# Optimization experiments

Hardware: AMD Instinct MI355X
Metric: run time of the kernel (lower is better)

The kernel has to match this reference:

```python
import jax, jax.numpy as jnp
import numpy as np

B = 512
D_IN = 64
D_MODEL = 768
DEPTH = 24
D_INNER = 1536   # expand=2 * d_model
D_STATE = 16
D_CONV = 4
DT_RANK = 48     # ceil(d_model/16)


def setup_inputs() -> dict:
    key = jax.random.key(0)
    ks = jax.random.split(key, 12)
    s = 0.02
    x_t = jax.random.normal(ks[0], (B, 1, D_IN), dtype=jnp.float32)
    in_w = jax.random.normal(ks[1], (D_MODEL, D_IN), dtype=jnp.float32) * s
    in_b = jnp.zeros((D_MODEL,), jnp.float32)
    xz_w = jax.random.normal(ks[2], (DEPTH, 2 * D_INNER, D_MODEL), dtype=jnp.float32) * s
    conv_w = jax.random.normal(ks[3], (DEPTH, D_INNER, D_CONV), dtype=jnp.float32) * s
    conv_b = jnp.zeros((DEPTH, D_INNER), jnp.float32)
    xproj_w = jax.random.normal(ks[4], (DEPTH, DT_RANK + 2 * D_STATE, D_INNER), dtype=jnp.float32) * s
    dtproj_w = jax.random.normal(ks[5], (DEPTH, D_INNER, DT_RANK), dtype=jnp.float32) * s
    # dt bias initialized so softplus(dt) ~ [1e-3, 1e-1], as in mamba_ssm
    dtproj_b = jax.random.uniform(ks[6], (DEPTH, D_INNER), minval=-4.6, maxval=-2.3)
    # A = arange(1, d_state+1) per channel -> A_log = log(A)
    A_log = jnp.broadcast_to(jnp.log(jnp.arange(1, D_STATE + 1, dtype=jnp.float32)),
                             (DEPTH, D_INNER, D_STATE)).copy()
    D = jnp.ones((DEPTH, D_INNER), jnp.float32)
    outproj_w = jax.random.normal(ks[7], (DEPTH, D_MODEL, D_INNER), dtype=jnp.float32) * s
    conv_state = jax.random.normal(ks[8], (DEPTH, B, D_INNER, D_CONV), dtype=jnp.float32) * 0.1
    ssm_state = jax.random.normal(ks[9], (DEPTH, B, D_INNER, D_STATE), dtype=jnp.float32) * 0.1
    ln_g = jnp.ones((D_MODEL,), jnp.float32)
    ln_b = jnp.zeros((D_MODEL,), jnp.float32)
    return dict(x_t=x_t, in_w=in_w, in_b=in_b, xz_w=xz_w, conv_w=conv_w, conv_b=conv_b,
                xproj_w=xproj_w, dtproj_w=dtproj_w, dtproj_b=dtproj_b, A_log=A_log, D=D,
                outproj_w=outproj_w, conv_state=conv_state, ssm_state=ssm_state,
                ln_g=ln_g, ln_b=ln_b)


def _layer_step(h, layer):
    """One Mamba selective-scan decode step for a single layer. h: (B, D_INNER*... wait (B, d_model))"""
    (xz_w, conv_w, conv_b, xproj_w, dtproj_w, dtproj_b, A_log, Dp, outproj_w, cs, ss) = layer
    xz = h @ xz_w.T                                  # (B, 2*d_inner)
    x, z = jnp.split(xz, 2, axis=-1)                 # (B, d_inner) each
    # causal conv1d cache update: shift left, append new token
    cs = jnp.concatenate([cs[..., 1:], x[..., None]], axis=-1)   # (B, d_inner, d_conv)
    x = jnp.sum(cs * conv_w[None], axis=-1) + conv_b             # (B, d_inner)
    x = jax.nn.silu(x)
    xdb = x @ xproj_w.T                              # (B, dt_rank + 2*d_state)
    dt = xdb[:, :DT_RANK] @ dtproj_w.T               # (B, d_inner)
    Bm = xdb[:, DT_RANK:DT_RANK + D_STATE]           # (B, d_state)
    C = xdb[:, DT_RANK + D_STATE:]                   # (B, d_state)
    dt = jax.nn.softplus(dt + dtproj_b)
    A = -jnp.exp(A_log)                              # (d_inner, d_state)
    dA = jnp.exp(dt[:, :, None] * A[None])           # (B, d_inner, d_state)
    ss = ss * dA + (dt * x)[:, :, None] * Bm[:, None, :]
    y = jnp.einsum('bdn,bn->bd', ss, C) + Dp * x
    y = y * jax.nn.silu(z)
    h = y @ outproj_w.T                              # (B, d_model)
    return h, None


def reference(x_t, in_w, in_b, xz_w, conv_w, conv_b, xproj_w, dtproj_w, dtproj_b,
              A_log, D, outproj_w, conv_state, ssm_state, ln_g, ln_b):
    h = x_t[:, 0, :] @ in_w.T + in_b                 # (B, d_model)
    h, _ = jax.lax.scan(_layer_step, h,
                        (xz_w, conv_w, conv_b, xproj_w, dtproj_w, dtproj_b,
                         A_log, D, outproj_w, conv_state, ssm_state))
    mu = jnp.mean(h, axis=-1, keepdims=True)
    var = jnp.var(h, axis=-1, keepdims=True)
    h = (h - mu) / jnp.sqrt(var + 1e-5) * ln_g + ln_b
    return h[:, None, :]                             # (B, 1, d_model)
```

## Files before the change

kernel.cpp:

```cpp
#include <hip/hip_runtime.h>
#include <cstdint>
#include <cstddef>

#define BATCH 512
#define D_IN 64
#define D_MODEL 768
#define DEPTH 24
#define D_INNER 1536
#define D_STATE 16
#define D_CONV 4
#define DT_RANK 48
#define XDB_DIM 80

typedef __bf16 bf16x8 __attribute__((ext_vector_type(8)));
typedef unsigned short ushortx8 __attribute__((ext_vector_type(8)));
typedef float f32x4 __attribute__((ext_vector_type(4)));
typedef unsigned short ushort_t;

#define XZW_N ((size_t)2 * D_INNER * D_MODEL)
#define OPW_N ((size_t)D_MODEL * D_INNER)
#define XZ_ALL ((long)DEPTH * (long)(XZW_N / 8))
#define OP_ALL ((long)DEPTH * (long)(OPW_N / 8))
#define AN_ALL ((long)DEPTH * D_INNER * D_STATE / 8)

__device__ __forceinline__ float sigmoidf_(float v) { return 1.f / (1.f + __expf(-v)); }

__device__ __forceinline__ void split1(float f, unsigned short& h, unsigned short& l) {
    unsigned int u = __float_as_uint(f);
    unsigned int uh = u & 0xffff0000u;
    h = (unsigned short)(uh >> 16);
    float r = f - __uint_as_float(uh);
    l = (unsigned short)(__float_as_uint(r) >> 16);
}

__device__ __forceinline__ void split8(const float* s, ushort_t* hi, ushort_t* lo) {
    float4 A4 = *(const float4*)s;
    float4 B4 = *(const float4*)(s + 4);
    float f[8] = {A4.x, A4.y, A4.z, A4.w, B4.x, B4.y, B4.z, B4.w};
    ushortx8 h, l;
#pragma unroll
    for (int j = 0; j < 8; ++j) {
        unsigned short hh, ll;
        split1(f[j], hh, ll);
        h[j] = hh; l[j] = ll;
    }
    *(ushortx8*)hi = h;
    *(ushortx8*)lo = l;
}

__global__ __launch_bounds__(256) void k_prep(
    const float* __restrict__ xz_w, const float* __restrict__ op_w,
    const float* __restrict__ A_log,
    ushort_t* __restrict__ xzw_hi, ushort_t* __restrict__ xzw_lo,
    ushort_t* __restrict__ opw_hi, ushort_t* __restrict__ opw_lo,
    float* __restrict__ Aneg)
{
    const long total = XZ_ALL + OP_ALL + AN_ALL;
    long g = (long)blockIdx.x * 256 + threadIdx.x;
    const long stride = (long)gridDim.x * 256;
    for (; g < total; g += stride) {
        if (g < XZ_ALL) {
            split8(xz_w + g * 8, xzw_hi + g * 8, xzw_lo + g * 8);
        } else if (g < XZ_ALL + OP_ALL) {
            const long r = g - XZ_ALL;
            split8(op_w + r * 8, opw_hi + r * 8, opw_lo + r * 8);
        } else {
            const long r = g - XZ_ALL - OP_ALL;
            const float* s = A_log + r * 8;
            float* d = Aneg + r * 8;
#pragma unroll
            for (int j = 0; j < 8; ++j) d[j] = -__expf(s[j]);
        }
    }
}

__global__ __launch_bounds__(256) void k_inproj(
    const float* __restrict__ A, const float* __restrict__ W,
    const float* __restrict__ bias,
    ushort_t* __restrict__ Chi, ushort_t* __restrict__ Clo)
{
    __shared__ float As[16][68];
    __shared__ float Ws[16][68];
    const int tid = threadIdx.x;
    const int tx = tid & 15, ty = tid >> 4;
    const int bn0 = blockIdx.x * 64, bm0 = blockIdx.y * 64;
    float acc[4][4] = {};
    for (int k0 = 0; k0 < D_IN; k0 += 16) {
        int r = tid >> 2, c = (tid & 3) << 2;
        float4 a4 = *(const float4*)(A + (size_t)(bm0 + r) * D_IN + k0 + c);
        As[c + 0][r] = a4.x; As[c + 1][r] = a4.y;
        As[c + 2][r] = a4.z; As[c + 3][r] = a4.w;
        float4 w4 = *(const float4*)(W + (size_t)(bn0 + r) * D_IN + k0 + c);
        Ws[c + 0][r] = w4.x; Ws[c + 1][r] = w4.y;
        Ws[c + 2][r] = w4.z; Ws[c + 3][r] = w4.w;
        __syncthreads();
#pragma unroll
        for (int kk = 0; kk < 16; ++kk) {
            float af[4], wf[4];
#pragma unroll
            for (int i = 0; i < 4; ++i) af[i] = As[kk][ty * 4 + i];
#pragma unroll
            for (int j = 0; j < 4; ++j) wf[j] = Ws[kk][tx * 4 + j];
#pragma unroll
            for (int i = 0; i < 4; ++i)
#pragma unroll
                for (int j = 0; j < 4; ++j) acc[i][j] += af[i] * wf[j];
        }
        __syncthreads();
    }
#pragma unroll
    for (int i = 0; i < 4; ++i) {
        const int bb = bm0 + ty * 4 + i;
#pragma unroll
        for (int j = 0; j < 4; ++j) {
            const int n = bn0 + tx * 4 + j;
            float v = acc[i][j] + bias[n];
            const size_t idx = (size_t)bb * D_MODEL + n;
            unsigned short hh, ll;
            split1(v, hh, ll);
            Chi[idx] = hh;
            Clo[idx] = ll;
        }
    }
}

template<int MODE>
__global__ __launch_bounds__(256) void k_gemm(
    const ushort_t* __restrict__ Ahi, const ushort_t* __restrict__ Alo,
    const ushort_t* __restrict__ Whi, const ushort_t* __restrict__ Wlo,
    float* __restrict__ xout, float* __restrict__ gout,
    float* __restrict__ hout, ushort_t* __restrict__ Chi, ushort_t* __restrict__ Clo,
    const float* __restrict__ conv_state, const float* __restrict__ conv_w,
    const float* __restrict__ conv_b)
{
    constexpr int K = (MODE == 0) ? D_MODEL : D_INNER;
    constexpr int nk = K / 32;
    const int bid = blockIdx.x;
    int c, r;
    if (MODE == 0) {
        c = (bid & 7) + ((bid >> 6) << 3);
        r = (bid >> 3) & 7;
    } else {
        if (bid < 64) { c = bid & 7; r = bid >> 3; }
        else { const int j = bid - 64; c = 8 + (j & 3); r = j >> 2; }
    }
    const int bn0 = c * 64, bm0 = r * 64;

    __shared__ __align__(16) unsigned short As[2][64 * 64];
    __shared__ __align__(16) unsigned short Bs[2][64 * 64];

    const int t = threadIdx.x;
    const int sr = t >> 2, s0 = t & 3;
    const int lane = t & 63, wv = t >> 6;
    const int wm = wv >> 1, wn = wv & 1;
    const int ln15 = lane & 15, kq = lane >> 4;

    const ushort_t* Ah = Ahi + (size_t)(bm0 + sr) * K + s0 * 8;
    const ushort_t* Al = Alo + (size_t)(bm0 + sr) * K + s0 * 8;
    const ushort_t* Wh = Whi + (size_t)(bn0 + sr) * K + s0 * 8;
    const ushort_t* Wl = Wlo + (size_t)(bn0 + sr) * K + s0 * 8;

    f32x4 acc[2][2];
#pragma unroll
    for (int m = 0; m < 2; ++m)
#pragma unroll
        for (int n = 0; n < 2; ++n) acc[m][n] = (f32x4){0.f, 0.f, 0.f, 0.f};

    const int sw = sr & 7;
    auto stage = [&](ushortx8 hi, ushortx8 lo, unsigned short* S) {
        *(ushortx8*)&S[sr * 64 + ((s0 ^ sw) << 3)] = hi;
        *(ushortx8*)&S[sr * 64 + (((s0 + 4) ^ sw) << 3)] = lo;
    };

    ushortx8 pah = *(const ushortx8*)Ah;
    ushortx8 pal = *(const ushortx8*)Al;
    ushortx8 pwh = *(const ushortx8*)Wh;
    ushortx8 pwl = *(const ushortx8*)Wl;
    stage(pah, pal, As[0]);
    stage(pwh, pwl, Bs[0]);

    for (int kb = 0; kb < nk; ++kb) {
        __syncthreads();
        const int cur = kb & 1;
        if (kb + 1 < nk) {
            const int ko = (kb + 1) << 5;
            pah = *(const ushortx8*)(Ah + ko);
            pal = *(const ushortx8*)(Al + ko);
            pwh = *(const ushortx8*)(Wh + ko);
            pwl = *(const ushortx8*)(Wl + ko);
        }
        bf16x8 ah[2], al2[2], bh[2], bl[2];
#pragma unroll
        for (int m = 0; m < 2; ++m) {
            const int rr = wm * 32 + m * 16 + ln15;
            const int base = rr * 64;
            const int rs = rr & 7;
            ah[m]  = __builtin_bit_cast(bf16x8, *(ushortx8*)&As[cur][base + ((kq ^ rs) << 3)]);
            al2[m] = __builtin_bit_cast(bf16x8, *(ushortx8*)&As[cur][base + (((kq + 4) ^ rs) << 3)]);
        }
#pragma unroll
        for (int n = 0; n < 2; ++n) {
            const int rr = wn * 32 + n * 16 + ln15;
            const int base = rr * 64;
            const int rs = rr & 7;
            bh[n] = __builtin_bit_cast(bf16x8, *(ushortx8*)&Bs[cur][base + ((kq ^ rs) << 3)]);
            bl[n] = __builtin_bit_cast(bf16x8, *(ushortx8*)&Bs[cur][base + (((kq + 4) ^ rs) << 3)]);
        }
#pragma unroll
        for (int m = 0; m < 2; ++m)
#pragma unroll
            for (int n = 0; n < 2; ++n) {
                acc[m][n] = __builtin_amdgcn_mfma_f32_16x16x32_bf16(ah[m],  bh[n], acc[m][n], 0, 0, 0);
                acc[m][n] = __builtin_amdgcn_mfma_f32_16x16x32_bf16(ah[m],  bl[n], acc[m][n], 0, 0, 0);
                acc[m][n] = __builtin_amdgcn_mfma_f32_16x16x32_bf16(al2[m], bh[n], acc[m][n], 0, 0, 0);
            }
        if (kb + 1 < nk) {
            stage(pah, pal, As[cur ^ 1]);
            stage(pwh, pwl, Bs[cur ^ 1]);
        }
    }

#pragma unroll
    for (int m = 0; m < 2; ++m) {
#pragma unroll
        for (int n = 0; n < 2; ++n) {
            const int col = bn0 + wn * 32 + n * 16 + ln15;
            const int row0 = bm0 + wm * 32 + m * 16 + kq * 4;
            f32x4 v = acc[m][n];
            if (MODE == 0) {
                if (col < D_INNER) {
                    const float4 cwv = *(const float4*)(conv_w + (size_t)col * 4);
                    const float cbv = conv_b[col];
#pragma unroll
                    for (int j = 0; j < 4; ++j) {
                        const int row = row0 + j;
                        const float4 csv = *(const float4*)(conv_state + ((size_t)row * D_INNER + col) * 4);
                        float cc = csv.y * cwv.x + csv.z * cwv.y + csv.w * cwv.z
                                 + v[j] * cwv.w + cbv;
                        xout[(size_t)row * D_INNER + col] = cc * sigmoidf_(cc);
                    }
                } else {
#pragma unroll
                    for (int j = 0; j < 4; ++j) {
                        float zv = v[j];
                        gout[(size_t)(row0 + j) * D_INNER + (col - D_INNER)] = zv * sigmoidf_(zv);
                    }
                }
            } else {
#pragma unroll
                for (int j = 0; j < 4; ++j) {
                    const size_t idx = (size_t)(row0 + j) * D_MODEL + col;
                    float val = v[j];
                    hout[idx] = val;
                    unsigned short hh, ll;
                    split1(val, hh, ll);
                    Chi[idx] = hh;
                    Clo[idx] = ll;
                }
            }
        }
    }
}

__global__ __launch_bounds__(256) void k_bc(
    const float* __restrict__ x, const float* __restrict__ g,
    const float* __restrict__ xproj_w, const float* __restrict__ dtproj_w,
    const float* __restrict__ dtproj_b, const float* __restrict__ Aneg_l,
    const float* __restrict__ Dp, const float* __restrict__ ssm,
    ushort_t* __restrict__ yhi, ushort_t* __restrict__ ylo)
{
    __shared__ __align__(16) float xs0[D_INNER];
    __shared__ __align__(16) float xs1[D_INNER];
    __shared__ float xdb0[XDB_DIM];
    __shared__ float xdb1[XDB_DIM];
    const int tid = threadIdx.x;
    const int b0 = blockIdx.x * 2, b1 = b0 + 1;

    {
        const float4* xr0 = (const float4*)(x + (size_t)b0 * D_INNER);
        const float4* xr1 = (const float4*)(x + (size_t)b1 * D_INNER);
        float4* d0 = (float4*)xs0; float4* d1 = (float4*)xs1;
        for (int i = tid; i < D_INNER / 4; i += 256) { d0[i] = xr0[i]; d1[i] = xr1[i]; }
    }
    __syncthreads();

    const int lane = tid & 63, wv = tid >> 6;
    const float4* xs40 = (const float4*)xs0;
    const float4* xs41 = (const float4*)xs1;
    for (int n = wv; n < XDB_DIM; n += 4) {
        const float4* wr = (const float4*)(xproj_w + (size_t)n * D_INNER);
        float s0 = 0.f, s1 = 0.f;
#pragma unroll
        for (int j = 0; j < D_INNER / 4 / 64; ++j) {
            float4 w = wr[lane + 64 * j];
            float4 u = xs40[lane + 64 * j];
            float4 q = xs41[lane + 64 * j];
            s0 += w.x * u.x + w.y * u.y + w.z * u.z + w.w * u.w;
            s1 += w.x * q.x + w.y * q.y + w.z * q.z + w.w * q.w;
        }
#pragma unroll
        for (int off = 32; off > 0; off >>= 1) { s0 += __shfl_xor(s0, off); s1 += __shfl_xor(s1, off); }
        if (lane == 0) { xdb0[n] = s0; xdb1[n] = s1; }
    }
    __syncthreads();

    float B0[16], C0[16], B1[16], C1[16];
#pragma unroll
    for (int n = 0; n < 16; ++n) {
        B0[n] = xdb0[DT_RANK + n]; C0[n] = xdb0[DT_RANK + 16 + n];
        B1[n] = xdb1[DT_RANK + n]; C1[n] = xdb1[DT_RANK + 16 + n];
    }

    for (int d = tid; d < D_INNER; d += 256) {
        const float4* dtw = (const float4*)(dtproj_w + (size_t)d * DT_RANK);
        float s0 = 0.f, s1 = 0.f;
#pragma unroll
        for (int j = 0; j < DT_RANK / 4; ++j) {
            float4 w = dtw[j];
            s0 += w.x * xdb0[4*j] + w.y * xdb0[4*j+1] + w.z * xdb0[4*j+2] + w.w * xdb0[4*j+3];
            s1 += w.x * xdb1[4*j] + w.y * xdb1[4*j+1] + w.z * xdb1[4*j+2] + w.w * xdb1[4*j+3];
        }
        const float bb = dtproj_b[d];
        s0 += bb; s1 += bb;
        float dt0 = fmaxf(s0, 0.f) + log1pf(__expf(-fabsf(s0)));
        float dt1 = fmaxf(s1, 0.f) + log1pf(__expf(-fabsf(s1)));
        const float xv0 = xs0[d], xv1 = xs1[d];
        const float dtx0 = dt0 * xv0, dtx1 = dt1 * xv1;
        const float4* anp = (const float4*)(Aneg_l + (size_t)d * D_STATE);
        const float4* sp0 = (const float4*)(ssm + ((size_t)b0 * D_INNER + d) * D_STATE);
        const float4* sp1 = (const float4*)(ssm + ((size_t)b1 * D_INNER + d) * D_STATE);
        float y0 = 0.f, y1 = 0.f;
#pragma unroll
        for (int q = 0; q < 4; ++q) {
            float4 an = anp[q];
            float4 u = sp0[q];
            float4 w = sp1[q];
            float e;
            e = __expf(dt0 * an.x); y0 += (u.x * e + dtx0 * B0[4*q+0]) * C0[4*q+0];
            e = __expf(dt0 * an.y); y0 += (u.y * e + dtx0 * B0[4*q+1]) * C0[4*q+1];
            e = __expf(dt0 * an.z); y0 += (u.z * e + dtx0 * B0[4*q+2]) * C0[4*q+2];
            e = __expf(dt0 * an.w); y0 += (u.w * e + dtx0 * B0[4*q+3]) * C0[4*q+3];
            e = __expf(dt1 * an.x); y1 += (w.x * e + dtx1 * B1[4*q+0]) * C1[4*q+0];
            e = __expf(dt1 * an.y); y1 += (w.y * e + dtx1 * B1[4*q+1]) * C1[4*q+1];
            e = __expf(dt1 * an.z); y1 += (w.z * e + dtx1 * B1[4*q+2]) * C1[4*q+2];
            e = __expf(dt1 * an.w); y1 += (w.w * e + dtx1 * B1[4*q+3]) * C1[4*q+3];
        }
        const float dv = Dp[d];
        y0 += dv * xv0; y1 += dv * xv1;
        const float o0 = y0 * g[(size_t)b0 * D_INNER + d];
        const float o1 = y1 * g[(size_t)b1 * D_INNER + d];
        unsigned short hh, ll;
        split1(o0, hh, ll);
        yhi[(size_t)b0 * D_INNER + d] = hh; ylo[(size_t)b0 * D_INNER + d] = ll;
        split1(o1, hh, ll);
        yhi[(size_t)b1 * D_INNER + d] = hh; ylo[(size_t)b1 * D_INNER + d] = ll;
    }
}

__global__ __launch_bounds__(256) void k_ln(
    const float* __restrict__ h, const float* __restrict__ gam,
    const float* __restrict__ bet, float* __restrict__ out)
{
    const int b = blockIdx.x;
    const int tid = threadIdx.x;
    float v[3];
#pragma unroll
    for (int j = 0; j < 3; ++j) v[j] = h[(size_t)b * D_MODEL + tid + j * 256];
    float s = v[0] + v[1] + v[2];
    float s2 = v[0] * v[0] + v[1] * v[1] + v[2] * v[2];
#pragma unroll
    for (int off = 32; off > 0; off >>= 1) {
        s += __shfl_xor(s, off);
        s2 += __shfl_xor(s2, off);
    }
    __shared__ float red[8];
    const int lane = tid & 63, wv = tid >> 6;
    if (lane == 0) { red[wv] = s; red[4 + wv] = s2; }
    __syncthreads();
    s = red[0] + red[1] + red[2] + red[3];
    s2 = red[4] + red[5] + red[6] + red[7];
    const float mu = s * (1.f / D_MODEL);
    const float var = s2 * (1.f / D_MODEL) - mu * mu;
    const float inv = 1.f / sqrtf(var + 1e-5f);
#pragma unroll
    for (int j = 0; j < 3; ++j) {
        int c = tid + j * 256;
        out[(size_t)b * D_MODEL + c] = (v[j] - mu) * inv * gam[c] + bet[c];
    }
}

extern "C" void kernel_launch(void* const* d_in, const int* in_sizes, int n_in,
                              void* d_out, int out_size, void* d_ws, size_t ws_size,
                              hipStream_t stream)
{
    const float* x_t        = (const float*)d_in[0];
    const float* in_w       = (const float*)d_in[1];
    const float* in_b       = (const float*)d_in[2];
    const float* xz_w       = (const float*)d_in[3];
    const float* conv_w     = (const float*)d_in[4];
    const float* conv_b     = (const float*)d_in[5];
    const float* xproj_w    = (const float*)d_in[6];
    const float* dtproj_w   = (const float*)d_in[7];
    const float* dtproj_b   = (const float*)d_in[8];
    const float* A_log      = (const float*)d_in[9];
    const float* Dvec       = (const float*)d_in[10];
    const float* outproj_w  = (const float*)d_in[11];
    const float* conv_state = (const float*)d_in[12];
    const float* ssm_state  = (const float*)d_in[13];
    const float* ln_g       = (const float*)d_in[14];
    const float* ln_b       = (const float*)d_in[15];

    float* ws = (float*)d_ws;
    float* h    = ws;
    float* x    = h + (size_t)BATCH * D_MODEL;
    float* g    = x + (size_t)BATCH * D_INNER;
    float* Aneg = g + (size_t)BATCH * D_INNER;
    ushort_t* h_hi = (ushort_t*)(Aneg + (size_t)DEPTH * D_INNER * D_STATE);
    ushort_t* h_lo = h_hi + (size_t)BATCH * D_MODEL;
    ushort_t* y_hi = h_lo + (size_t)BATCH * D_MODEL;
    ushort_t* y_lo = y_hi + (size_t)BATCH * D_INNER;
    ushort_t* xzw_hi = y_lo + (size_t)BATCH * D_INNER;
    ushort_t* xzw_lo = xzw_hi + (size_t)DEPTH * XZW_N;
    ushort_t* opw_hi = xzw_lo + (size_t)DEPTH * XZW_N;
    ushort_t* opw_lo = opw_hi + (size_t)DEPTH * OPW_N;

    dim3 blk(256);

    k_prep<<<dim3(2048), blk, 0, stream>>>(
        xz_w, outproj_w, A_log, xzw_hi, xzw_lo, opw_hi, opw_lo, Aneg);

    k_inproj<<<dim3(12, 8), blk, 0, stream>>>(x_t, in_w, in_b, h_hi, h_lo);

    for (int l = 0; l < DEPTH; ++l) {
        const ushort_t* xzh = xzw_hi + (size_t)l * XZW_N;
        const ushort_t* xzl = xzw_lo + (size_t)l * XZW_N;
        const ushort_t* oph = opw_hi + (size_t)l * OPW_N;
        const ushort_t* opl = opw_lo + (size_t)l * OPW_N;
        const float* csl = conv_state + (size_t)l * BATCH * D_INNER * D_CONV;
        const float* cwl = conv_w + (size_t)l * D_INNER * D_CONV;
        const float* cbl = conv_b + (size_t)l * D_INNER;
        const float* xpl = xproj_w + (size_t)l * XDB_DIM * D_INNER;
        const float* dwl = dtproj_w + (size_t)l * D_INNER * DT_RANK;
        const float* dbl = dtproj_b + (size_t)l * D_INNER;
        const float* anl = Aneg + (size_t)l * D_INNER * D_STATE;
        const float* dpl = Dvec + (size_t)l * D_INNER;
        const float* ssl = ssm_state + (size_t)l * BATCH * D_INNER * D_STATE;

        k_gemm<0><<<dim3(384), blk, 0, stream>>>(
            h_hi, h_lo, xzh, xzl, x, g, nullptr, nullptr, nullptr,
            csl, cwl, cbl);

        k_bc<<<dim3(256), blk, 0, stream>>>(
            x, g, xpl, dwl, dbl, anl, dpl, ssl, y_hi, y_lo);

        k_gemm<1><<<dim3(96), blk, 0, stream>>>(
            y_hi, y_lo, oph, opl, nullptr, nullptr, h, h_hi, h_lo,
            nullptr, nullptr, nullptr);
    }

    k_ln<<<dim3(BATCH), blk, 0, stream>>>(h, ln_g, ln_b, (float*)d_out);
}
```

Before: 2.498 ms.

## Fuse all layers into a persistent cooperative kernel with XCD-local batch barriers

Replaces the 73 per-layer kernel launches with a single cooperative persistent kernel of 512 blocks. Each block reads its XCC id so that batch-row groups of 64 rows stay within one XCD, and only the blocks sharing those rows sync through a per-group counter barrier plus a cache invalidate. If the XCD placement is uneven it falls back to a grid-wide barrier, and if the cooperative launch fails it runs the original multi-kernel path. The aim is to remove launch overhead and inter-kernel gaps, at the cost of idle blocks in narrow phases and spin-wait barriers.

```diff
diff --git a/kernel.cpp b/kernel.cpp
--- a/kernel.cpp
+++ b/kernel.cpp
@@ -11,6 +11,18 @@
 #define D_CONV 4
 #define DT_RANK 48
 #define XDB_DIM 80
+#define GRID 512
+#define NTHREADS 256
+
+#define XCC_GETREG_IMM (20 | (3 << 11))
+
+#define CTR_GCNT 0
+#define CTR_GO   32
+#define CTR_GBAR 64
+#define CTR_GGEN 96
+#define CTR_RANK 128
+#define CTR_XBAR 384
+#define CTR_TOTAL 1024
 
 typedef __bf16 bf16x8 __attribute__((ext_vector_type(8)));
 typedef unsigned short ushortx8 __attribute__((ext_vector_type(8)));
@@ -22,6 +34,15 @@
 #define XZ_ALL ((long)DEPTH * (long)(XZW_N / 8))
 #define OP_ALL ((long)DEPTH * (long)(OPW_N / 8))
 #define AN_ALL ((long)DEPTH * D_INNER * D_STATE / 8)
+
+struct Args {
+    const float *x_t, *in_w, *in_b, *conv_state, *conv_w, *conv_b;
+    const float *xproj_w, *dtproj_w, *dtproj_b, *Dvec, *ssm_state, *ln_g, *ln_b;
+    float *h, *x, *g, *Aneg, *out;
+    ushort_t *h_hi, *h_lo, *y_hi, *y_lo;
+    ushort_t *xzw_hi, *xzw_lo, *opw_hi, *opw_lo;
+    unsigned *ctr;
+};
 
 __device__ __forceinline__ float sigmoidf_(float v) { return 1.f / (1.f + __expf(-v)); }
 
@@ -46,6 +67,10 @@
     }
     *(ushortx8*)hi = h;
     *(ushortx8*)lo = l;
+}
+
+__global__ __launch_bounds__(64) void k_init(unsigned* ctr) {
+    for (int i = threadIdx.x; i < CTR_TOTAL; i += 64) ctr[i] = 0u;
 }
 
 __global__ __launch_bounds__(256) void k_prep(
@@ -56,16 +81,16 @@
     float* __restrict__ Aneg)
 {
     const long total = XZ_ALL + OP_ALL + AN_ALL;
-    long g = (long)blockIdx.x * 256 + threadIdx.x;
+    long gg = (long)blockIdx.x * 256 + threadIdx.x;
     const long stride = (long)gridDim.x * 256;
-    for (; g < total; g += stride) {
-        if (g < XZ_ALL) {
-            split8(xz_w + g * 8, xzw_hi + g * 8, xzw_lo + g * 8);
-        } else if (g < XZ_ALL + OP_ALL) {
-            const long r = g - XZ_ALL;
+    for (; gg < total; gg += stride) {
+        if (gg < XZ_ALL) {
+            split8(xz_w + gg * 8, xzw_hi + gg * 8, xzw_lo + gg * 8);
+        } else if (gg < XZ_ALL + OP_ALL) {
+            const long r = gg - XZ_ALL;
             split8(op_w + r * 8, opw_hi + r * 8, opw_lo + r * 8);
         } else {
-            const long r = g - XZ_ALL - OP_ALL;
+            const long r = gg - XZ_ALL - OP_ALL;
             const float* s = A_log + r * 8;
             float* d = Aneg + r * 8;
 #pragma unroll
@@ -74,23 +99,20 @@
     }
 }
 
-__global__ __launch_bounds__(256) void k_inproj(
-    const float* __restrict__ A, const float* __restrict__ W,
-    const float* __restrict__ bias,
-    ushort_t* __restrict__ Chi, ushort_t* __restrict__ Clo)
-{
-    __shared__ float As[16][68];
-    __shared__ float Ws[16][68];
+
+__device__ void dev_inproj(const Args& a, int g, int rk, char* smem) {
+    float (*As)[68] = (float (*)[68])smem;
+    float (*Ws)[68] = (float (*)[68])(smem + 16 * 68 * 4);
     const int tid = threadIdx.x;
     const int tx = tid & 15, ty = tid >> 4;
-    const int bn0 = blockIdx.x * 64, bm0 = blockIdx.y * 64;
+    const int bm0 = g * 64, bn0 = rk * 64;
     float acc[4][4] = {};
     for (int k0 = 0; k0 < D_IN; k0 += 16) {
         int r = tid >> 2, c = (tid & 3) << 2;
-        float4 a4 = *(const float4*)(A + (size_t)(bm0 + r) * D_IN + k0 + c);
+        float4 a4 = *(const float4*)(a.x_t + (size_t)(bm0 + r) * D_IN + k0 + c);
         As[c + 0][r] = a4.x; As[c + 1][r] = a4.y;
         As[c + 2][r] = a4.z; As[c + 3][r] = a4.w;
-        float4 w4 = *(const float4*)(W + (size_t)(bn0 + r) * D_IN + k0 + c);
+        float4 w4 = *(const float4*)(a.in_w + (size_t)(bn0 + r) * D_IN + k0 + c);
         Ws[c + 0][r] = w4.x; Ws[c + 1][r] = w4.y;
         Ws[c + 2][r] = w4.z; Ws[c + 3][r] = w4.w;
         __syncthreads();
@@ -114,40 +136,33 @@
 #pragma unroll
         for (int j = 0; j < 4; ++j) {
             const int n = bn0 + tx * 4 + j;
-            float v = acc[i][j] + bias[n];
+            float v = acc[i][j] + a.in_b[n];
             const size_t idx = (size_t)bb * D_MODEL + n;
             unsigned short hh, ll;
             split1(v, hh, ll);
-            Chi[idx] = hh;
-            Clo[idx] = ll;
+            a.h_hi[idx] = hh;
+            a.h_lo[idx] = ll;
         }
     }
 }
 
 template<int MODE>
-__global__ __launch_bounds__(256) void k_gemm(
-    const ushort_t* __restrict__ Ahi, const ushort_t* __restrict__ Alo,
-    const ushort_t* __restrict__ Whi, const ushort_t* __restrict__ Wlo,
-    float* __restrict__ xout, float* __restrict__ gout,
-    float* __restrict__ hout, ushort_t* __restrict__ Chi, ushort_t* __restrict__ Clo,
-    const float* __restrict__ conv_state, const float* __restrict__ conv_w,
-    const float* __restrict__ conv_b)
-{
+__device__ void dev_gemm(const Args& a, int l, int g, int rk, char* smem) {
     constexpr int K = (MODE == 0) ? D_MODEL : D_INNER;
     constexpr int nk = K / 32;
-    const int bid = blockIdx.x;
-    int c, r;
+    const int bm0 = g * 64, bn0 = rk * 64;
+    const ushort_t *Ahi, *Alo, *Whi, *Wlo;
     if (MODE == 0) {
-        c = (bid & 7) + ((bid >> 6) << 3);
-        r = (bid >> 3) & 7;
+        Ahi = a.h_hi; Alo = a.h_lo;
+        Whi = a.xzw_hi + (size_t)l * XZW_N;
+        Wlo = a.xzw_lo + (size_t)l * XZW_N;
     } else {
-        if (bid < 64) { c = bid & 7; r = bid >> 3; }
-        else { const int j = bid - 64; c = 8 + (j & 3); r = j >> 2; }
-    }
-    const int bn0 = c * 64, bm0 = r * 64;
-
-    __shared__ __align__(16) unsigned short As[2][64 * 64];
-    __shared__ __align__(16) unsigned short Bs[2][64 * 64];
+        Ahi = a.y_hi; Alo = a.y_lo;
+        Whi = a.opw_hi + (size_t)l * OPW_N;
+        Wlo = a.opw_lo + (size_t)l * OPW_N;
+    }
+    unsigned short* As = (unsigned short*)smem;
+    unsigned short* Bs = (unsigned short*)(smem + 16384);
 
     const int t = threadIdx.x;
     const int sr = t >> 2, s0 = t & 3;
@@ -176,8 +191,8 @@
     ushortx8 pal = *(const ushortx8*)Al;
     ushortx8 pwh = *(const ushortx8*)Wh;
     ushortx8 pwl = *(const ushortx8*)Wl;
-    stage(pah, pal, As[0]);
-    stage(pwh, pwl, Bs[0]);
+    stage(pah, pal, As);
+    stage(pwh, pwl, Bs);
 
     for (int kb = 0; kb < nk; ++kb) {
         __syncthreads();
@@ -193,18 +208,18 @@
 #pragma unroll
         for (int m = 0; m < 2; ++m) {
             const int rr = wm * 32 + m * 16 + ln15;
-            const int base = rr * 64;
+            const int base = cur * 4096 + rr * 64;
             const int rs = rr & 7;
-            ah[m]  = __builtin_bit_cast(bf16x8, *(ushortx8*)&As[cur][base + ((kq ^ rs) << 3)]);
-            al2[m] = __builtin_bit_cast(bf16x8, *(ushortx8*)&As[cur][base + (((kq + 4) ^ rs) << 3)]);
+            ah[m]  = __builtin_bit_cast(bf16x8, *(ushortx8*)&As[base + ((kq ^ rs) << 3)]);
+            al2[m] = __builtin_bit_cast(bf16x8, *(ushortx8*)&As[base + (((kq + 4) ^ rs) << 3)]);
         }
 #pragma unroll
         for (int n = 0; n < 2; ++n) {
             const int rr = wn * 32 + n * 16 + ln15;
-            const int base = rr * 64;
+            const int base = cur * 4096 + rr * 64;
             const int rs = rr & 7;
-            bh[n] = __builtin_bit_cast(bf16x8, *(ushortx8*)&Bs[cur][base + ((kq ^ rs) << 3)]);
-            bl[n] = __builtin_bit_cast(bf16x8, *(ushortx8*)&Bs[cur][base + (((kq + 4) ^ rs) << 3)]);
+            bh[n] = __builtin_bit_cast(bf16x8, *(ushortx8*)&Bs[base + ((kq ^ rs) << 3)]);
+            bl[n] = __builtin_bit_cast(bf16x8, *(ushortx8*)&Bs[base + (((kq + 4) ^ rs) << 3)]);
         }
 #pragma unroll
         for (int m = 0; m < 2; ++m)
@@ -215,8 +230,8 @@
                 acc[m][n] = __builtin_amdgcn_mfma_f32_16x16x32_bf16(al2[m], bh[n], acc[m][n], 0, 0, 0);
             }
         if (kb + 1 < nk) {
-            stage(pah, pal, As[cur ^ 1]);
-            stage(pwh, pwl, Bs[cur ^ 1]);
+            stage(pah, pal, As + (cur ^ 1) * 4096);
+            stage(pwh, pwl, Bs + (cur ^ 1) * 4096);
         }
     }
 
@@ -228,22 +243,25 @@
             const int row0 = bm0 + wm * 32 + m * 16 + kq * 4;
             f32x4 v = acc[m][n];
             if (MODE == 0) {
+                const float* csl = a.conv_state + (size_t)l * BATCH * D_INNER * D_CONV;
+                const float* cwl = a.conv_w + (size_t)l * D_INNER * D_CONV;
+                const float* cbl = a.conv_b + (size_t)l * D_INNER;
                 if (col < D_INNER) {
-                    const float4 cwv = *(const float4*)(conv_w + (size_t)col * 4);
-                    const float cbv = conv_b[col];
+                    const float4 cwv = *(const float4*)(cwl + (size_t)col * 4);
+                    const float cbv = cbl[col];
 #pragma unroll
                     for (int j = 0; j < 4; ++j) {
                         const int row = row0 + j;
-                        const float4 csv = *(const float4*)(conv_state + ((size_t)row * D_INNER + col) * 4);
+                        const float4 csv = *(const float4*)(csl + ((size_t)row * D_INNER + col) * 4);
                         float cc = csv.y * cwv.x + csv.z * cwv.y + csv.w * cwv.z
                                  + v[j] * cwv.w + cbv;
-                        xout[(size_t)row * D_INNER + col] = cc * sigmoidf_(cc);
+                        a.x[(size_t)row * D_INNER + col] = cc * sigmoidf_(cc);
                     }
                 } else {
 #pragma unroll
                     for (int j = 0; j < 4; ++j) {
                         float zv = v[j];
-                        gout[(size_t)(row0 + j) * D_INNER + (col - D_INNER)] = zv * sigmoidf_(zv);
+                        a.g[(size_t)(row0 + j) * D_INNER + (col - D_INNER)] = zv * sigmoidf_(zv);
                     }
                 }
             } else {
@@ -251,36 +269,36 @@
                 for (int j = 0; j < 4; ++j) {
                     const size_t idx = (size_t)(row0 + j) * D_MODEL + col;
                     float val = v[j];
-                    hout[idx] = val;
+                    a.h[idx] = val;
                     unsigned short hh, ll;
                     split1(val, hh, ll);
-                    Chi[idx] = hh;
-                    Clo[idx] = ll;
+                    a.h_hi[idx] = hh;
+                    a.h_lo[idx] = ll;
                 }
             }
         }
     }
 }
 
-__global__ __launch_bounds__(256) void k_bc(
-    const float* __restrict__ x, const float* __restrict__ g,
-    const float* __restrict__ xproj_w, const float* __restrict__ dtproj_w,
-    const float* __restrict__ dtproj_b, const float* __restrict__ Aneg_l,
-    const float* __restrict__ Dp, const float* __restrict__ ssm,
-    ushort_t* __restrict__ yhi, ushort_t* __restrict__ ylo)
-{
-    __shared__ __align__(16) float xs0[D_INNER];
-    __shared__ __align__(16) float xs1[D_INNER];
-    __shared__ float xdb0[XDB_DIM];
-    __shared__ float xdb1[XDB_DIM];
+__device__ void dev_bc(const Args& a, int l, int g, int rk, char* smem) {
+    float* xs0 = (float*)smem;
+    float* xs1 = xs0 + D_INNER;
+    float* xdb0 = xs1 + D_INNER;
+    float* xdb1 = xdb0 + XDB_DIM;
     const int tid = threadIdx.x;
-    const int b0 = blockIdx.x * 2, b1 = b0 + 1;
+    const int b0 = g * 64 + rk * 2, b1 = b0 + 1;
+    const float* xpl = a.xproj_w + (size_t)l * XDB_DIM * D_INNER;
+    const float* dwl = a.dtproj_w + (size_t)l * D_INNER * DT_RANK;
+    const float* dbl = a.dtproj_b + (size_t)l * D_INNER;
+    const float* anl = a.Aneg + (size_t)l * D_INNER * D_STATE;
+    const float* dpl = a.Dvec + (size_t)l * D_INNER;
+    const float* ssl = a.ssm_state + (size_t)l * BATCH * D_INNER * D_STATE;
 
     {
-        const float4* xr0 = (const float4*)(x + (size_t)b0 * D_INNER);
-        const float4* xr1 = (const float4*)(x + (size_t)b1 * D_INNER);
+        const float4* xr0 = (const float4*)(a.x + (size_t)b0 * D_INNER);
+        const float4* xr1 = (const float4*)(a.x + (size_t)b1 * D_INNER);
         float4* d0 = (float4*)xs0; float4* d1 = (float4*)xs1;
-        for (int i = tid; i < D_INNER / 4; i += 256) { d0[i] = xr0[i]; d1[i] = xr1[i]; }
+        for (int i = tid; i < D_INNER / 4; i += NTHREADS) { d0[i] = xr0[i]; d1[i] = xr1[i]; }
     }
     __syncthreads();
 
@@ -288,7 +306,7 @@
     const float4* xs40 = (const float4*)xs0;
     const float4* xs41 = (const float4*)xs1;
     for (int n = wv; n < XDB_DIM; n += 4) {
-        const float4* wr = (const float4*)(xproj_w + (size_t)n * D_INNER);
+        const float4* wr = (const float4*)(xpl + (size_t)n * D_INNER);
         float s0 = 0.f, s1 = 0.f;
 #pragma unroll
         for (int j = 0; j < D_INNER / 4 / 64; ++j) {
@@ -311,8 +329,8 @@
         B1[n] = xdb1[DT_RANK + n]; C1[n] = xdb1[DT_RANK + 16 + n];
     }
 
-    for (int d = tid; d < D_INNER; d += 256) {
-        const float4* dtw = (const float4*)(dtproj_w + (size_t)d * DT_RANK);
+    for (int d = tid; d < D_INNER; d += NTHREADS) {
+        const float4* dtw = (const float4*)(dwl + (size_t)d * DT_RANK);
         float s0 = 0.f, s1 = 0.f;
 #pragma unroll
         for (int j = 0; j < DT_RANK / 4; ++j) {
@@ -320,15 +338,15 @@
             s0 += w.x * xdb0[4*j] + w.y * xdb0[4*j+1] + w.z * xdb0[4*j+2] + w.w * xdb0[4*j+3];
             s1 += w.x * xdb1[4*j] + w.y * xdb1[4*j+1] + w.z * xdb1[4*j+2] + w.w * xdb1[4*j+3];
         }
-        const float bb = dtproj_b[d];
+        const float bb = dbl[d];
         s0 += bb; s1 += bb;
         float dt0 = fmaxf(s0, 0.f) + log1pf(__expf(-fabsf(s0)));
         float dt1 = fmaxf(s1, 0.f) + log1pf(__expf(-fabsf(s1)));
         const float xv0 = xs0[d], xv1 = xs1[d];
         const float dtx0 = dt0 * xv0, dtx1 = dt1 * xv1;
-        const float4* anp = (const float4*)(Aneg_l + (size_t)d * D_STATE);
-        const float4* sp0 = (const float4*)(ssm + ((size_t)b0 * D_INNER + d) * D_STATE);
-        const float4* sp1 = (const float4*)(ssm + ((size_t)b1 * D_INNER + d) * D_STATE);
+        const float4* anp = (const float4*)(anl + (size_t)d * D_STATE);
+        const float4* sp0 = (const float4*)(ssl + ((size_t)b0 * D_INNER + d) * D_STATE);
+        const float4* sp1 = (const float4*)(ssl + ((size_t)b1 * D_INNER + d) * D_STATE);
         float y0 = 0.f, y1 = 0.f;
 #pragma unroll
         for (int q = 0; q < 4; ++q) {
@@ -345,27 +363,25 @@
             e = __expf(dt1 * an.z); y1 += (w.z * e + dtx1 * B1[4*q+2]) * C1[4*q+2];
             e = __expf(dt1 * an.w); y1 += (w.w * e + dtx1 * B1[4*q+3]) * C1[4*q+3];
         }
-        const float dv = Dp[d];
+        const float dv = dpl[d];
         y0 += dv * xv0; y1 += dv * xv1;
-        const float o0 = y0 * g[(size_t)b0 * D_INNER + d];
-        const float o1 = y1 * g[(size_t)b1 * D_INNER + d];
+        const float o0 = y0 * a.g[(size_t)b0 * D_INNER + d];
+        const float o1 = y1 * a.g[(size_t)b1 * D_INNER + d];
         unsigned short hh, ll;
         split1(o0, hh, ll);
-        yhi[(size_t)b0 * D_INNER + d] = hh; ylo[(size_t)b0 * D_INNER + d] = ll;
+        a.y_hi[(size_t)b0 * D_INNER + d] = hh; a.y_lo[(size_t)b0 * D_INNER + d] = ll;
         split1(o1, hh, ll);
-        yhi[(size_t)b1 * D_INNER + d] = hh; ylo[(size_t)b1 * D_INNER + d] = ll;
-    }
-}
-
-__global__ __launch_bounds__(256) void k_ln(
-    const float* __restrict__ h, const float* __restrict__ gam,
-    const float* __restrict__ bet, float* __restrict__ out)
-{
-    const int b = blockIdx.x;
+        a.y_hi[(size_t)b1 * D_INNER + d] = hh; a.y_lo[(size_t)b1 * D_INNER + d] = ll;
+    }
+}
+
+__device__ void dev_ln(const Args& a, int g, int rk, char* smem) {
+    float* red = (float*)smem;
     const int tid = threadIdx.x;
+    const int b = g * 64 + rk;
     float v[3];
 #pragma unroll
-    for (int j = 0; j < 3; ++j) v[j] = h[(size_t)b * D_MODEL + tid + j * 256];
+    for (int j = 0; j < 3; ++j) v[j] = a.h[(size_t)b * D_MODEL + tid + j * 256];
     float s = v[0] + v[1] + v[2];
     float s2 = v[0] * v[0] + v[1] * v[1] + v[2] * v[2];
 #pragma unroll
@@ -373,7 +389,6 @@
         s += __shfl_xor(s, off);
         s2 += __shfl_xor(s2, off);
     }
-    __shared__ float red[8];
     const int lane = tid & 63, wv = tid >> 6;
     if (lane == 0) { red[wv] = s; red[4 + wv] = s2; }
     __syncthreads();
@@ -385,33 +400,115 @@
 #pragma unroll
     for (int j = 0; j < 3; ++j) {
         int c = tid + j * 256;
-        out[(size_t)b * D_MODEL + c] = (v[j] - mu) * inv * gam[c] + bet[c];
-    }
+        a.out[(size_t)b * D_MODEL + c] = (v[j] - mu) * inv * a.ln_g[c] + a.ln_b[c];
+    }
+}
+
+__global__ __launch_bounds__(NTHREADS, 2) void persist(Args a) {
+    __shared__ __align__(16) char smem[57344];
+    __shared__ unsigned s_vx, s_rk, s_gr, s_mode;
+    if (threadIdx.x == 0) {
+        unsigned vx = __builtin_amdgcn_s_getreg(XCC_GETREG_IMM) & 7u;
+        unsigned rk = __hip_atomic_fetch_add(&a.ctr[CTR_RANK + vx * 32], 1u,
+                                             __ATOMIC_RELAXED, __HIP_MEMORY_SCOPE_AGENT);
+        asm volatile("s_waitcnt vmcnt(0)" ::: "memory");
+        unsigned gr = __hip_atomic_fetch_add(&a.ctr[CTR_GCNT], 1u,
+                                             __ATOMIC_RELAXED, __HIP_MEMORY_SCOPE_AGENT);
+        if (gr == GRID - 1) {
+            bool good = true;
+            for (int v = 0; v < 8; ++v)
+                good = good && (__hip_atomic_load(&a.ctr[CTR_RANK + v * 32],
+                        __ATOMIC_RELAXED, __HIP_MEMORY_SCOPE_AGENT) == 64u);
+            __hip_atomic_store(&a.ctr[CTR_GO], good ? 3u : 2u,
+                               __ATOMIC_RELAXED, __HIP_MEMORY_SCOPE_AGENT);
+        }
+        unsigned go;
+        while ((go = __hip_atomic_load(&a.ctr[CTR_GO], __ATOMIC_RELAXED,
+                                       __HIP_MEMORY_SCOPE_AGENT)) < 2u)
+            __builtin_amdgcn_s_sleep(32);
+        s_vx = vx; s_rk = rk; s_gr = gr; s_mode = go;
+    }
+    __syncthreads();
+    const bool good = (s_mode == 3u);
+    const int g  = good ? (int)s_vx : (int)(s_gr >> 6);
+    const int rk = good ? (int)s_rk : (int)(s_gr & 63u);
+    unsigned* xc = &a.ctr[CTR_XBAR + g * 32];
+    unsigned xtgt = 0, ggen = 0;
+
+    auto bar = [&]() {
+        __syncthreads();
+        if (good) {
+            xtgt += 64;
+            if (threadIdx.x == 0) {
+                __hip_atomic_fetch_add(xc, 1u, __ATOMIC_RELAXED, __HIP_MEMORY_SCOPE_AGENT);
+                while (__hip_atomic_load(xc, __ATOMIC_RELAXED,
+                                         __HIP_MEMORY_SCOPE_AGENT) < xtgt)
+                    __builtin_amdgcn_s_sleep(32);
+            }
+            __syncthreads();
+            asm volatile("buffer_inv sc0" ::: "memory");
+        } else {
+            ggen += 1;
+            if (threadIdx.x == 0) {
+                __builtin_amdgcn_fence(__ATOMIC_RELEASE, "agent");
+                unsigned old = __hip_atomic_fetch_add(&a.ctr[CTR_GBAR], 1u,
+                        __ATOMIC_RELAXED, __HIP_MEMORY_SCOPE_AGENT);
+                if (old == ggen * GRID - 1) {
+                    __hip_atomic_store(&a.ctr[CTR_GGEN], ggen,
+                            __ATOMIC_RELAXED, __HIP_MEMORY_SCOPE_AGENT);
+                } else {
+                    while (__hip_atomic_load(&a.ctr[CTR_GGEN], __ATOMIC_RELAXED,
+                                             __HIP_MEMORY_SCOPE_AGENT) < ggen)
+                        __builtin_amdgcn_s_sleep(32);
+                }
+                __builtin_amdgcn_fence(__ATOMIC_ACQUIRE, "agent");
+            }
+            __syncthreads();
+        }
+    };
+
+    if (rk < 12) dev_inproj(a, g, rk, smem);
+    bar();
+
+    for (int l = 0; l < DEPTH; ++l) {
+        if (rk < 48) dev_gemm<0>(a, l, g, rk, smem);
+        bar();
+        if (rk < 32) dev_bc(a, l, g, rk, smem);
+        bar();
+        if (rk < 12) dev_gemm<1>(a, l, g, rk, smem);
+        bar();
+    }
+    dev_ln(a, g, rk, smem);
+}
+
+__global__ __launch_bounds__(NTHREADS) void k_inproj(Args a) {
+    __shared__ __align__(16) char smem[32768];
+    dev_inproj(a, blockIdx.x / 12, blockIdx.x % 12, smem);
+}
+__global__ __launch_bounds__(NTHREADS) void k_xz(Args a, int l) {
+    __shared__ __align__(16) char smem[32768];
+    dev_gemm<0>(a, l, blockIdx.x / 48, blockIdx.x % 48, smem);
+}
+__global__ __launch_bounds__(NTHREADS) void k_bc(Args a, int l) {
+    __shared__ __align__(16) char smem[32768];
+    dev_bc(a, l, blockIdx.x / 32, blockIdx.x % 32, smem);
+}
+__global__ __launch_bounds__(NTHREADS) void k_op(Args a, int l) {
+    __shared__ __align__(16) char smem[32768];
+    dev_gemm<1>(a, l, blockIdx.x / 12, blockIdx.x % 12, smem);
+}
+__global__ __launch_bounds__(NTHREADS) void k_ln(Args a) {
+    __shared__ __align__(16) char smem[32768];
+    dev_ln(a, blockIdx.x / 64, blockIdx.x % 64, smem);
 }
 
 extern "C" void kernel_launch(void* const* d_in, const int* in_sizes, int n_in,
                               void* d_out, int out_size, void* d_ws, size_t ws_size,
                               hipStream_t stream)
 {
-    const float* x_t        = (const float*)d_in[0];
-    const float* in_w       = (const float*)d_in[1];
-    const float* in_b       = (const float*)d_in[2];
-    const float* xz_w       = (const float*)d_in[3];
-    const float* conv_w     = (const float*)d_in[4];
-    const float* conv_b     = (const float*)d_in[5];
-    const float* xproj_w    = (const float*)d_in[6];
-    const float* dtproj_w   = (const float*)d_in[7];
-    const float* dtproj_b   = (const float*)d_in[8];
-    const float* A_log      = (const float*)d_in[9];
-    const float* Dvec       = (const float*)d_in[10];
-    const float* outproj_w  = (const float*)d_in[11];
-    const float* conv_state = (const float*)d_in[12];
-    const float* ssm_state  = (const float*)d_in[13];
-    const float* ln_g       = (const float*)d_in[14];
-    const float* ln_b       = (const float*)d_in[15];
-
-    float* ws = (float*)d_ws;
-    float* h    = ws;
+    char* wsb = (char*)d_ws;
+    unsigned* ctr = (unsigned*)wsb;
+    float* h    = (float*)(wsb + 4096);
     float* x    = h + (size_t)BATCH * D_MODEL;
     float* g    = x + (size_t)BATCH * D_INNER;
     float* Aneg = g + (size_t)BATCH * D_INNER;
@@ -424,39 +521,47 @@
     ushort_t* opw_hi = xzw_lo + (size_t)DEPTH * XZW_N;
     ushort_t* opw_lo = opw_hi + (size_t)DEPTH * OPW_N;
 
-    dim3 blk(256);
-
+    Args args;
+    args.x_t        = (const float*)d_in[0];
+    args.in_w       = (const float*)d_in[1];
+    args.in_b       = (const float*)d_in[2];
+    const float* xz_w      = (const float*)d_in[3];
+    args.conv_w     = (const float*)d_in[4];
+    args.conv_b     = (const float*)d_in[5];
+    args.xproj_w    = (const float*)d_in[6];
+    args.dtproj_w   = (const float*)d_in[7];
+    args.dtproj_b   = (const float*)d_in[8];
+    const float* A_log     = (const float*)d_in[9];
+    args.Dvec       = (const float*)d_in[10];
+    const float* outproj_w = (const float*)d_in[11];
+    args.conv_state = (const float*)d_in[12];
+    args.ssm_state  = (const float*)d_in[13];
+    args.ln_g       = (const float*)d_in[14];
+    args.ln_b       = (const float*)d_in[15];
+    args.h = h; args.x = x; args.g = g; args.Aneg = Aneg;
+    args.out = (float*)d_out;
+    args.h_hi = h_hi; args.h_lo = h_lo; args.y_hi = y_hi; args.y_lo = y_lo;
+    args.xzw_hi = xzw_hi; args.xzw_lo = xzw_lo;
+    args.opw_hi = opw_hi; args.opw_lo = opw_lo;
+    args.ctr = ctr;
+
+    dim3 blk(NTHREADS);
+
+    k_init<<<dim3(1), dim3(64), 0, stream>>>(ctr);
     k_prep<<<dim3(2048), blk, 0, stream>>>(
         xz_w, outproj_w, A_log, xzw_hi, xzw_lo, opw_hi, opw_lo, Aneg);
 
-    k_inproj<<<dim3(12, 8), blk, 0, stream>>>(x_t, in_w, in_b, h_hi, h_lo);
-
-    for (int l = 0; l < DEPTH; ++l) {
-        const ushort_t* xzh = xzw_hi + (size_t)l * XZW_N;
-        const ushort_t* xzl = xzw_lo + (size_t)l * XZW_N;
-        const ushort_t* oph = opw_hi + (size_t)l * OPW_N;
-        const ushort_t* opl = opw_lo + (size_t)l * OPW_N;
-        const float* csl = conv_state + (size_t)l * BATCH * D_INNER * D_CONV;
-        const float* cwl = conv_w + (size_t)l * D_INNER * D_CONV;
-        const float* cbl = conv_b + (size_t)l * D_INNER;
-        const float* xpl = xproj_w + (size_t)l * XDB_DIM * D_INNER;
-        const float* dwl = dtproj_w + (size_t)l * D_INNER * DT_RANK;
-        const float* dbl = dtproj_b + (size_t)l * D_INNER;
-        const float* anl = Aneg + (size_t)l * D_INNER * D_STATE;
-        const float* dpl = Dvec + (size_t)l * D_INNER;
-        const float* ssl = ssm_state + (size_t)l * BATCH * D_INNER * D_STATE;
-
-        k_gemm<0><<<dim3(384), blk, 0, stream>>>(
-            h_hi, h_lo, xzh, xzl, x, g, nullptr, nullptr, nullptr,
-            csl, cwl, cbl);
-
-        k_bc<<<dim3(256), blk, 0, stream>>>(
-            x, g, xpl, dwl, dbl, anl, dpl, ssl, y_hi, y_lo);
-
-        k_gemm<1><<<dim3(96), blk, 0, stream>>>(
-            y_hi, y_lo, oph, opl, nullptr, nullptr, h, h_hi, h_lo,
-            nullptr, nullptr, nullptr);
-    }
-
-    k_ln<<<dim3(BATCH), blk, 0, stream>>>(h, ln_g, ln_b, (float*)d_out);
-}
+    void* kp[] = { &args };
+    hipError_t e = hipLaunchCooperativeKernel((const void*)persist, dim3(GRID),
+                                              dim3(NTHREADS), kp, 0, stream);
+    if (e != hipSuccess) {
+        (void)hipGetLastError();
+        k_inproj<<<dim3(96), blk, 0, stream>>>(args);
+        for (int l = 0; l < DEPTH; ++l) {
+            k_xz<<<dim3(384), blk, 0, stream>>>(args, l);
+            k_bc<<<dim3(256), blk, 0, stream>>>(args, l);
+            k_op<<<dim3(96), blk, 0, stream>>>(args, l);
+        }
+        k_ln<<<dim3(512), blk, 0, stream>>>(args);
+    }
+}
```

After: 4.027 ms. 61.2% more time.

## Pre-swizzle GEMM operands into MFMA fragment layout and load directly from global

Applied to the files above, without the earlier changes.

The weights (during prep) and the activations (in the producing kernels) are now written in a fragment-tiled layout that matches the 16x16x32 MFMA operand pattern. The GEMM kernel drops its shared-memory double buffering and barriers and reads each wave's fragments straight from global memory with coalesced 16-byte loads. This removes LDS staging and sync overhead. In exchange, each wave reloads operands that other waves in the block share, relying on cache, and there is no explicit prefetch to hide global latency.

```diff
diff --git a/kernel.cpp b/kernel.cpp
--- a/kernel.cpp
+++ b/kernel.cpp
@@ -19,9 +19,6 @@
 
 #define XZW_N ((size_t)2 * D_INNER * D_MODEL)
 #define OPW_N ((size_t)D_MODEL * D_INNER)
-#define XZ_ALL ((long)DEPTH * (long)(XZW_N / 8))
-#define OP_ALL ((long)DEPTH * (long)(OPW_N / 8))
-#define AN_ALL ((long)DEPTH * D_INNER * D_STATE / 8)
 
 __device__ __forceinline__ float sigmoidf_(float v) { return 1.f / (1.f + __expf(-v)); }
 
@@ -33,19 +30,9 @@
     l = (unsigned short)(__float_as_uint(r) >> 16);
 }
 
-__device__ __forceinline__ void split8(const float* s, ushort_t* hi, ushort_t* lo) {
-    float4 A4 = *(const float4*)s;
-    float4 B4 = *(const float4*)(s + 4);
-    float f[8] = {A4.x, A4.y, A4.z, A4.w, B4.x, B4.y, B4.z, B4.w};
-    ushortx8 h, l;
-#pragma unroll
-    for (int j = 0; j < 8; ++j) {
-        unsigned short hh, ll;
-        split1(f[j], hh, ll);
-        h[j] = hh; l[j] = ll;
-    }
-    *(ushortx8*)hi = h;
-    *(ushortx8*)lo = l;
+__device__ __forceinline__ size_t fl_idx(int row, int k, int Mtot) {
+    return ((size_t)(k >> 5) * (Mtot >> 4) + (row >> 4)) * 512
+         + (size_t)(((k >> 3) & 3) << 7) + ((row & 15) << 3) + (k & 7);
 }
 
 __global__ __launch_bounds__(256) void k_prep(
@@ -55,15 +42,42 @@
     ushort_t* __restrict__ opw_hi, ushort_t* __restrict__ opw_lo,
     float* __restrict__ Aneg)
 {
+    const long XZ_ALL = (long)DEPTH * (long)(XZW_N / 8);
+    const long OP_ALL = (long)DEPTH * (long)(OPW_N / 8);
+    const long AN_ALL = (long)DEPTH * D_INNER * D_STATE / 8;
     const long total = XZ_ALL + OP_ALL + AN_ALL;
     long g = (long)blockIdx.x * 256 + threadIdx.x;
     const long stride = (long)gridDim.x * 256;
     for (; g < total; g += stride) {
         if (g < XZ_ALL) {
-            split8(xz_w + g * 8, xzw_hi + g * 8, xzw_lo + g * 8);
+            const int l = (int)(g / (XZW_N / 8));
+            const long gl = (g - (long)l * (XZW_N / 8)) * 8;
+            const int n = (int)(gl / D_MODEL), k0 = (int)(gl % D_MODEL);
+            const float* s = xz_w + (size_t)l * XZW_N + gl;
+            const size_t dst = (size_t)l * XZW_N + fl_idx(n, k0, 2 * D_INNER);
+            float4 A4 = *(const float4*)s;
+            float4 B4 = *(const float4*)(s + 4);
+            float f[8] = {A4.x, A4.y, A4.z, A4.w, B4.x, B4.y, B4.z, B4.w};
+            ushortx8 h, lo;
+#pragma unroll
+            for (int j = 0; j < 8; ++j) { unsigned short hh, ll; split1(f[j], hh, ll); h[j] = hh; lo[j] = ll; }
+            *(ushortx8*)(xzw_hi + dst) = h;
+            *(ushortx8*)(xzw_lo + dst) = lo;
         } else if (g < XZ_ALL + OP_ALL) {
             const long r = g - XZ_ALL;
-            split8(op_w + r * 8, opw_hi + r * 8, opw_lo + r * 8);
+            const int l = (int)(r / (OPW_N / 8));
+            const long gl = (r - (long)l * (OPW_N / 8)) * 8;
+            const int n = (int)(gl / D_INNER), k0 = (int)(gl % D_INNER);
+            const float* s = op_w + (size_t)l * OPW_N + gl;
+            const size_t dst = (size_t)l * OPW_N + fl_idx(n, k0, D_MODEL);
+            float4 A4 = *(const float4*)s;
+            float4 B4 = *(const float4*)(s + 4);
+            float f[8] = {A4.x, A4.y, A4.z, A4.w, B4.x, B4.y, B4.z, B4.w};
+            ushortx8 h, lo;
+#pragma unroll
+            for (int j = 0; j < 8; ++j) { unsigned short hh, ll; split1(f[j], hh, ll); h[j] = hh; lo[j] = ll; }
+            *(ushortx8*)(opw_hi + dst) = h;
+            *(ushortx8*)(opw_lo + dst) = lo;
         } else {
             const long r = g - XZ_ALL - OP_ALL;
             const float* s = A_log + r * 8;
@@ -115,9 +129,9 @@
         for (int j = 0; j < 4; ++j) {
             const int n = bn0 + tx * 4 + j;
             float v = acc[i][j] + bias[n];
-            const size_t idx = (size_t)bb * D_MODEL + n;
             unsigned short hh, ll;
             split1(v, hh, ll);
+            const size_t idx = fl_idx(bb, n, BATCH);
             Chi[idx] = hh;
             Clo[idx] = ll;
         }
@@ -134,7 +148,11 @@
     const float* __restrict__ conv_b)
 {
     constexpr int K = (MODE == 0) ? D_MODEL : D_INNER;
-    constexpr int nk = K / 32;
+    constexpr int NK = K / 32;
+    constexpr int NT = (MODE == 0) ? 2 * D_INNER : D_MODEL;
+    constexpr size_t ASTEP = (size_t)(BATCH >> 4) * 512;
+    constexpr size_t WSTEP = (size_t)(NT >> 4) * 512;
+
     const int bid = blockIdx.x;
     int c, r;
     if (MODE == 0) {
@@ -146,19 +164,17 @@
     }
     const int bn0 = c * 64, bm0 = r * 64;
 
-    __shared__ __align__(16) unsigned short As[2][64 * 64];
-    __shared__ __align__(16) unsigned short Bs[2][64 * 64];
-
     const int t = threadIdx.x;
-    const int sr = t >> 2, s0 = t & 3;
     const int lane = t & 63, wv = t >> 6;
     const int wm = wv >> 1, wn = wv & 1;
     const int ln15 = lane & 15, kq = lane >> 4;
 
-    const ushort_t* Ah = Ahi + (size_t)(bm0 + sr) * K + s0 * 8;
-    const ushort_t* Al = Alo + (size_t)(bm0 + sr) * K + s0 * 8;
-    const ushort_t* Wh = Whi + (size_t)(bn0 + sr) * K + s0 * 8;
-    const ushort_t* Wl = Wlo + (size_t)(bn0 + sr) * K + s0 * 8;
+    const size_t aoff = (size_t)((bm0 + wm * 32) >> 4) * 512 + lane * 8;
+    const size_t woff = (size_t)((bn0 + wn * 32) >> 4) * 512 + lane * 8;
+    const ushort_t* pah = Ahi + aoff;
+    const ushort_t* pal = Alo + aoff;
+    const ushort_t* pwh = Whi + woff;
+    const ushort_t* pwl = Wlo + woff;
 
     f32x4 acc[2][2];
 #pragma unroll
@@ -166,58 +182,27 @@
 #pragma unroll
         for (int n = 0; n < 2; ++n) acc[m][n] = (f32x4){0.f, 0.f, 0.f, 0.f};
 
-    const int sw = sr & 7;
-    auto stage = [&](ushortx8 hi, ushortx8 lo, unsigned short* S) {
-        *(ushortx8*)&S[sr * 64 + ((s0 ^ sw) << 3)] = hi;
-        *(ushortx8*)&S[sr * 64 + (((s0 + 4) ^ sw) << 3)] = lo;
-    };
-
-    ushortx8 pah = *(const ushortx8*)Ah;
-    ushortx8 pal = *(const ushortx8*)Al;
-    ushortx8 pwh = *(const ushortx8*)Wh;
-    ushortx8 pwl = *(const ushortx8*)Wl;
-    stage(pah, pal, As[0]);
-    stage(pwh, pwl, Bs[0]);
-
-    for (int kb = 0; kb < nk; ++kb) {
-        __syncthreads();
-        const int cur = kb & 1;
-        if (kb + 1 < nk) {
-            const int ko = (kb + 1) << 5;
-            pah = *(const ushortx8*)(Ah + ko);
-            pal = *(const ushortx8*)(Al + ko);
-            pwh = *(const ushortx8*)(Wh + ko);
-            pwl = *(const ushortx8*)(Wl + ko);
-        }
-        bf16x8 ah[2], al2[2], bh[2], bl[2];
+#pragma unroll 2
+    for (int ks = 0; ks < NK; ++ks) {
+        bf16x8 ah[2], al[2], bh[2], bl[2];
 #pragma unroll
         for (int m = 0; m < 2; ++m) {
-            const int rr = wm * 32 + m * 16 + ln15;
-            const int base = rr * 64;
-            const int rs = rr & 7;
-            ah[m]  = __builtin_bit_cast(bf16x8, *(ushortx8*)&As[cur][base + ((kq ^ rs) << 3)]);
-            al2[m] = __builtin_bit_cast(bf16x8, *(ushortx8*)&As[cur][base + (((kq + 4) ^ rs) << 3)]);
+            ah[m] = __builtin_bit_cast(bf16x8, *(const ushortx8*)(pah + ks * ASTEP + m * 512));
+            al[m] = __builtin_bit_cast(bf16x8, *(const ushortx8*)(pal + ks * ASTEP + m * 512));
         }
 #pragma unroll
         for (int n = 0; n < 2; ++n) {
-            const int rr = wn * 32 + n * 16 + ln15;
-            const int base = rr * 64;
-            const int rs = rr & 7;
-            bh[n] = __builtin_bit_cast(bf16x8, *(ushortx8*)&Bs[cur][base + ((kq ^ rs) << 3)]);
-            bl[n] = __builtin_bit_cast(bf16x8, *(ushortx8*)&Bs[cur][base + (((kq + 4) ^ rs) << 3)]);
+            bh[n] = __builtin_bit_cast(bf16x8, *(const ushortx8*)(pwh + ks * WSTEP + n * 512));
+            bl[n] = __builtin_bit_cast(bf16x8, *(const ushortx8*)(pwl + ks * WSTEP + n * 512));
         }
 #pragma unroll
         for (int m = 0; m < 2; ++m)
 #pragma unroll
             for (int n = 0; n < 2; ++n) {
-                acc[m][n] = __builtin_amdgcn_mfma_f32_16x16x32_bf16(ah[m],  bh[n], acc[m][n], 0, 0, 0);
-                acc[m][n] = __builtin_amdgcn_mfma_f32_16x16x32_bf16(ah[m],  bl[n], acc[m][n], 0, 0, 0);
-                acc[m][n] = __builtin_amdgcn_mfma_f32_16x16x32_bf16(al2[m], bh[n], acc[m][n], 0, 0, 0);
+                acc[m][n] = __builtin_amdgcn_mfma_f32_16x16x32_bf16(ah[m], bh[n], acc[m][n], 0, 0, 0);
+                acc[m][n] = __builtin_amdgcn_mfma_f32_16x16x32_bf16(ah[m], bl[n], acc[m][n], 0, 0, 0);
+                acc[m][n] = __builtin_amdgcn_mfma_f32_16x16x32_bf16(al[m], bh[n], acc[m][n], 0, 0, 0);
             }
-        if (kb + 1 < nk) {
-            stage(pah, pal, As[cur ^ 1]);
-            stage(pwh, pwl, Bs[cur ^ 1]);
-        }
     }
 
 #pragma unroll
@@ -249,11 +234,11 @@
             } else {
 #pragma unroll
                 for (int j = 0; j < 4; ++j) {
-                    const size_t idx = (size_t)(row0 + j) * D_MODEL + col;
                     float val = v[j];
-                    hout[idx] = val;
+                    hout[(size_t)(row0 + j) * D_MODEL + col] = val;
                     unsigned short hh, ll;
                     split1(val, hh, ll);
+                    const size_t idx = fl_idx(row0 + j, col, BATCH);
                     Chi[idx] = hh;
                     Clo[idx] = ll;
                 }
@@ -351,9 +336,11 @@
         const float o1 = y1 * g[(size_t)b1 * D_INNER + d];
         unsigned short hh, ll;
         split1(o0, hh, ll);
-        yhi[(size_t)b0 * D_INNER + d] = hh; ylo[(size_t)b0 * D_INNER + d] = ll;
+        const size_t i0 = fl_idx(b0, d, BATCH);
+        yhi[i0] = hh; ylo[i0] = ll;
         split1(o1, hh, ll);
-        yhi[(size_t)b1 * D_INNER + d] = hh; ylo[(size_t)b1 * D_INNER + d] = ll;
+        const size_t i1 = fl_idx(b1, d, BATCH);
+        yhi[i1] = hh; ylo[i1] = ll;
     }
 }
 
```

After: 3.098 ms. 1.24x slower.
